# Kernel optimization log

Measured on AMD Instinct MI355X. Metric: run time of the kernel, lower is better.

The kernel has to match this reference:

```python
import jax, jax.numpy as jnp
import numpy as np

DIM = 1536
NUM_HEADS = 24
HEAD_DIM = DIM // NUM_HEADS
SCALE = HEAD_DIM ** -0.5
B, NX, NC = 2, 2048, 256


def setup_inputs() -> dict:
    key = jax.random.key(0)
    ks = jax.random.split(key, 12)
    s = 0.02
    return {
        "x": jax.random.normal(ks[0], (B, NX, DIM), jnp.float32),
        "c": jax.random.normal(ks[1], (B, NC, DIM), jnp.float32),
        "Wqkv_x": jax.random.normal(ks[2], (3 * DIM, DIM), jnp.float32) * s,
        "bqkv_x": jax.random.normal(ks[3], (3 * DIM,), jnp.float32) * s,
        "Wqkv_c": jax.random.normal(ks[4], (3 * DIM, DIM), jnp.float32) * s,
        "bqkv_c": jax.random.normal(ks[5], (3 * DIM,), jnp.float32) * s,
        "Wproj_x": jax.random.normal(ks[6], (DIM, DIM), jnp.float32) * s,
        "bproj_x": jax.random.normal(ks[7], (DIM,), jnp.float32) * s,
        "Wproj_c": jax.random.normal(ks[8], (DIM, DIM), jnp.float32) * s,
        "bproj_c": jax.random.normal(ks[9], (DIM,), jnp.float32) * s,
    }


def _qkv(t, W, b):
    # t: [B, N, C] -> q, k, v each [B, H, N, Dh]
    Bt, N, C = t.shape
    qkv = (t @ W.T + b).reshape(Bt, N, 3, NUM_HEADS, HEAD_DIM)
    qkv = jnp.transpose(qkv, (2, 0, 3, 1, 4))  # [3, B, H, N, Dh]
    return qkv[0], qkv[1], qkv[2]


def reference(x, c, Wqkv_x, bqkv_x, Wqkv_c, bqkv_c, Wproj_x, bproj_x, Wproj_c, bproj_c):
    q_x, k_x, v_x = _qkv(x, Wqkv_x, bqkv_x)
    q_c, k_c, v_c = _qkv(c, Wqkv_c, bqkv_c)
    q = jnp.concatenate([q_x, q_c], axis=2)  # [B, H, Nx+Nc, Dh]
    k = jnp.concatenate([k_x, k_c], axis=2)
    v = jnp.concatenate([v_x, v_c], axis=2)
    attn = jnp.einsum("bhnd,bhmd->bhnm", q, k) * SCALE
    attn = jax.nn.softmax(attn, axis=-1)
    out = jnp.einsum("bhnm,bhmd->bhnd", attn, v)  # [B, H, N, Dh]
    x_out = out[:, :, :NX]
    c_out = out[:, :, NX:]
    x_out = jnp.transpose(x_out, (0, 2, 1, 3)).reshape(x.shape[0], NX, DIM)
    c_out = jnp.transpose(c_out, (0, 2, 1, 3)).reshape(c.shape[0], NC, DIM)
    return (x_out @ Wproj_x.T + bproj_x, c_out @ Wproj_c.T + bproj_c)
```

## Files before the change

### kernel.cpp

```cpp
#include <hip/hip_runtime.h>
#include <stdint.h>

#define HNUM 24
#define DIMX 1536
#define NXT  2048
#define NCT  256
#define NTOT 2304
#define BB   2

typedef __attribute__((ext_vector_type(8))) short bf16x8;
typedef __attribute__((ext_vector_type(8))) _Float16 f16x8;
typedef __attribute__((ext_vector_type(4))) _Float16 f16x4;
typedef __attribute__((ext_vector_type(4))) float f32x4;
typedef __attribute__((ext_vector_type(4))) unsigned short u16x4;

#define AS1 __attribute__((address_space(1)))
#define AS3 __attribute__((address_space(3)))

__device__ __forceinline__ void glds16(const void* g, void* l) {
  __builtin_amdgcn_global_load_lds((AS1 void*)(uintptr_t)g, (AS3 void*)l, 16, 0, 0);
}

__device__ __forceinline__ unsigned short f2bf(float f) {
  unsigned int u = __float_as_uint(f);
  u += 0x7FFFu + ((u >> 16) & 1u);
  return (unsigned short)(u >> 16);
}

__device__ __forceinline__ bf16x8 ldfragB(const unsigned short* S, int row, int cc) {
  return *(const bf16x8*)(S + row * 64 + ((cc ^ (row & 7)) << 3));
}
__device__ __forceinline__ f16x8 ldfragH(const _Float16* S, int row, int cc) {
  return *(const f16x8*)(S + row * 64 + ((cc ^ (row & 7)) << 3));
}

struct CastDesc { const float* src; unsigned short* dst; int start4; };
struct CastArgs { CastDesc d[6]; int total4; };

__global__ __launch_bounds__(256) void cast_all(CastArgs a) {
  int i = blockIdx.x * 256 + threadIdx.x;
  if (i >= a.total4) return;
  int r = 0;
#pragma unroll
  for (int k = 1; k < 6; ++k) r += (i >= a.d[k].start4);
  int j = i - a.d[r].start4;
  float4 v = reinterpret_cast<const float4*>(a.d[r].src)[j];
  u16x4 o;
  o[0] = f2bf(v.x); o[1] = f2bf(v.y); o[2] = f2bf(v.z); o[3] = f2bf(v.w);
  reinterpret_cast<u16x4*>(a.d[r].dst)[j] = o;
}

__device__ __forceinline__ void gemm_mainloop(
    const unsigned short* __restrict__ Ablk,
    const unsigned short* __restrict__ Wblk,
    unsigned short* As, unsigned short* Bs, f32x4 acc[4][4]) {
  const int tid  = threadIdx.x;
  const int lane = tid & 63;
  const int quad = lane >> 4, l16 = lane & 15;
  const int wave = tid >> 6;
  const int wm = (wave >> 1) * 64, wo = (wave & 1) * 64;

  for (int k0 = 0; k0 < DIMX; k0 += 64) {
    __syncthreads();
#pragma unroll
    for (int p = 0; p < 4; ++p) {
      int c = p * 256 + tid;
      int row = c >> 3;
      int kc = ((c & 7) ^ (row & 7)) << 3;
      glds16(Ablk + (size_t)row * DIMX + k0 + kc, As + c * 8);
      glds16(Wblk + (size_t)row * DIMX + k0 + kc, Bs + c * 8);
    }
    __syncthreads();
#pragma unroll
    for (int kk = 0; kk < 64; kk += 32) {
      bf16x8 af[4], bf[4];
#pragma unroll
      for (int mb = 0; mb < 4; ++mb)
        af[mb] = ldfragB(As, wm + mb * 16 + l16, (kk >> 3) + quad);
#pragma unroll
      for (int ob = 0; ob < 4; ++ob)
        bf[ob] = ldfragB(Bs, wo + ob * 16 + l16, (kk >> 3) + quad);
#pragma unroll
      for (int mb = 0; mb < 4; ++mb)
#pragma unroll
        for (int ob = 0; ob < 4; ++ob)
          acc[mb][ob] = __builtin_amdgcn_mfma_f32_16x16x32_bf16(
              af[mb], bf[ob], acc[mb][ob], 0, 0, 0);
    }
  }
}

__global__ __launch_bounds__(256, 3) void gemm_qkv(
    const unsigned short* __restrict__ xbf, const unsigned short* __restrict__ cbf,
    const unsigned short* __restrict__ Wx, const unsigned short* __restrict__ Wc,
    const float* __restrict__ bx_, const float* __restrict__ bc_,
    unsigned short* __restrict__ Qb, unsigned short* __restrict__ Kb,
    _Float16* __restrict__ VTf) {
  __shared__ unsigned short Sh[2][128 * 64];
  unsigned short* As = Sh[0];
  unsigned short* Bs = Sh[1];

  const bool isC = blockIdx.y >= 32;
  const int yloc = isC ? (int)blockIdx.y - 32 : (int)blockIdx.y;
  const int tokShift = isC ? 8 : 11;
  const int seqOff = isC ? NXT : 0;
  const unsigned short* A = (isC ? cbf : xbf) + (size_t)yloc * 128 * DIMX;
  const unsigned short* W = (isC ? Wc : Wx) + (size_t)blockIdx.x * 128 * DIMX;
  const float* bias = isC ? bc_ : bx_;

  const f32x4 z4 = {0.f, 0.f, 0.f, 0.f};
  f32x4 acc[4][4];
#pragma unroll
  for (int i = 0; i < 4; ++i)
#pragma unroll
    for (int j = 0; j < 4; ++j) acc[i][j] = z4;

  gemm_mainloop(A, W, As, Bs, acc);

  const int tid = threadIdx.x, lane = tid & 63, wave = tid >> 6;
  const int quad = lane >> 4, l16 = lane & 15;
  const int wm = (wave >> 1) * 64, wo = (wave & 1) * 64;
  const int s = blockIdx.x / 12;
  const float QSC = 0.125f * 1.44269504088896340736f;

  float bv[4];
#pragma unroll
  for (int ob = 0; ob < 4; ++ob)
    bv[ob] = bias[blockIdx.x * 128 + wo + ob * 16 + l16];

  if (s < 2) {
#pragma unroll
    for (int ob = 0; ob < 4; ++ob) {
      int o = blockIdx.x * 128 + wo + ob * 16 + l16;
      int rem = o - s * DIMX;
      int h = rem >> 6, d = rem & 63;
#pragma unroll
      for (int mb = 0; mb < 4; ++mb) {
#pragma unroll
        for (int r = 0; r < 4; ++r) {
          int m = yloc * 128 + wm + mb * 16 + quad * 4 + r;
          int b = m >> tokShift;
          int n = seqOff + (m & ((1 << tokShift) - 1));
          size_t bh = (size_t)b * HNUM + h;
          float v = acc[mb][ob][r] + bv[ob];
          if (s == 0) Qb[(bh * NTOT + n) * 64 + d] = f2bf(v * QSC);
          else        Kb[(bh * NTOT + n) * 64 + d] = f2bf(v);
        }
      }
    }
  } else {
    _Float16* Ts = (_Float16*)Sh;
    __syncthreads();
#pragma unroll
    for (int ob = 0; ob < 4; ++ob) {
      int dloc = wo + ob * 16 + l16;
      int sw = (dloc & 15) << 3;
#pragma unroll
      for (int mb = 0; mb < 4; ++mb) {
        f16x4 pk;
#pragma unroll
        for (int r = 0; r < 4; ++r) pk[r] = (_Float16)(acc[mb][ob][r] + bv[ob]);
        int m0 = wm + mb * 16 + quad * 4;
        *(f16x4*)(Ts + dloc * 128 + (m0 ^ sw)) = pk;
      }
    }
    __syncthreads();
#pragma unroll
    for (int it = 0; it < 8; ++it) {
      int cth = it * 256 + tid;
      int d = cth >> 4;
      int m0 = (cth & 15) << 3;
      f16x8 val = *(const f16x8*)(Ts + d * 128 + (m0 ^ ((d & 15) << 3)));
      int dglob = (blockIdx.x - 24) * 128 + d;
      int h = dglob >> 6, dd = dglob & 63;
      int M = yloc * 128 + m0;
      int b = M >> tokShift;
      int n = seqOff + (M & ((1 << tokShift) - 1));
      *(f16x8*)(VTf + ((size_t)(b * HNUM + h) * 64 + dd) * NTOT + n) = val;
    }
  }
}

__global__ __launch_bounds__(256, 3) void gemm_proj(
    const unsigned short* __restrict__ AX, const unsigned short* __restrict__ AC,
    const unsigned short* __restrict__ Wx, const unsigned short* __restrict__ Wc,
    const float* __restrict__ bx_, const float* __restrict__ bc_,
    float* __restrict__ out) {
  __shared__ unsigned short As[128 * 64];
  __shared__ unsigned short Bs[128 * 64];

  const bool isC = blockIdx.y >= 32;
  const int yloc = isC ? (int)blockIdx.y - 32 : (int)blockIdx.y;
  const unsigned short* A = (isC ? AC : AX) + (size_t)yloc * 128 * DIMX;
  const unsigned short* W = (isC ? Wc : Wx) + (size_t)blockIdx.x * 128 * DIMX;
  const float* bias = isC ? bc_ : bx_;
  float* o_ = out + (isC ? (size_t)BB * NXT * DIMX : (size_t)0) +
              (size_t)yloc * 128 * DIMX;

  const f32x4 z4 = {0.f, 0.f, 0.f, 0.f};
  f32x4 acc[4][4];
#pragma unroll
  for (int i = 0; i < 4; ++i)
#pragma unroll
    for (int j = 0; j < 4; ++j) acc[i][j] = z4;

  gemm_mainloop(A, W, As, Bs, acc);

  const int lane = threadIdx.x & 63, wave = threadIdx.x >> 6;
  const int quad = lane >> 4, l16 = lane & 15;
  const int wm = (wave >> 1) * 64, wo = (wave & 1) * 64;

#pragma unroll
  for (int ob = 0; ob < 4; ++ob) {
    int o = blockIdx.x * 128 + wo + ob * 16 + l16;
    float bv = bias[o];
#pragma unroll
    for (int mb = 0; mb < 4; ++mb) {
#pragma unroll
      for (int r = 0; r < 4; ++r) {
        int m = wm + mb * 16 + quad * 4 + r;
        o_[(size_t)m * DIMX + o] = acc[mb][ob][r] + bv;
      }
    }
  }
}

__global__ __launch_bounds__(256, 3) void flash_attn(
    const unsigned short* __restrict__ Qb, const unsigned short* __restrict__ Kb,
    const _Float16* __restrict__ Vf,
    unsigned short* __restrict__ AX, unsigned short* __restrict__ AC) {
  __shared__ unsigned short Ks[64 * 64];
  __shared__ _Float16      Vs[64 * 64];
  __shared__ _Float16      Ps[4][32 * 72];

  const int tid = threadIdx.x, lane = tid & 63, wave = tid >> 6;
  const int quad = lane >> 4, l16 = lane & 15;
  const int bh = blockIdx.y;
  const int qbase = blockIdx.x * 128 + wave * 32;

  bf16x8 qf[2][2];
#pragma unroll
  for (int qb = 0; qb < 2; ++qb)
#pragma unroll
    for (int kh = 0; kh < 2; ++kh)
      qf[qb][kh] = *(const bf16x8*)(
          Qb + ((size_t)bh * NTOT + qbase + qb * 16 + l16) * 64 + kh * 32 + quad * 8);

  const f32x4 z4 = {0.f, 0.f, 0.f, 0.f};
  f32x4 acc[2][4];
  float lp[2][4];
#pragma unroll
  for (int qb = 0; qb < 2; ++qb) {
#pragma unroll
    for (int db = 0; db < 4; ++db) acc[qb][db] = z4;
#pragma unroll
    for (int r = 0; r < 4; ++r) lp[qb][r] = 0.f;
  }

  const size_t kbase = (size_t)bh * NTOT * 64;
  const size_t vbase = (size_t)bh * 64 * NTOT;
  _Float16* Pw = &Ps[wave][0];

  for (int kt = 0; kt < 36; ++kt) {
    const int kv0 = kt * 64;
    __syncthreads();
#pragma unroll
    for (int p = 0; p < 2; ++p) {
      int c = p * 256 + tid;
      int row = c >> 3;
      int kc = ((c & 7) ^ (row & 7)) << 3;
      glds16(Kb + kbase + (size_t)(kv0 + row) * 64 + kc, Ks + c * 8);
      glds16(Vf + vbase + (size_t)row * NTOT + kv0 + kc, Vs + c * 8);
    }
    __syncthreads();

    f32x4 s[2][4];
#pragma unroll
    for (int qb = 0; qb < 2; ++qb)
#pragma unroll
      for (int cb = 0; cb < 4; ++cb) s[qb][cb] = z4;
#pragma unroll
    for (int kh = 0; kh < 2; ++kh) {
      bf16x8 kf[4];
#pragma unroll
      for (int cb = 0; cb < 4; ++cb)
        kf[cb] = ldfragB(Ks, cb * 16 + l16, kh * 4 + quad);
#pragma unroll
      for (int qb = 0; qb < 2; ++qb)
#pragma unroll
        for (int cb = 0; cb < 4; ++cb)
          s[qb][cb] = __builtin_amdgcn_mfma_f32_16x16x32_bf16(
              qf[qb][kh], kf[cb], s[qb][cb], 0, 0, 0);
    }

#pragma unroll
    for (int qb = 0; qb < 2; ++qb)
#pragma unroll
      for (int cb = 0; cb < 4; ++cb)
#pragma unroll
        for (int r = 0; r < 4; ++r) {
          float pe = __builtin_amdgcn_exp2f(s[qb][cb][r]);
          lp[qb][r] += pe;
          Pw[(qb * 16 + quad * 4 + r) * 72 + cb * 16 + l16] = (_Float16)pe;
        }

#pragma unroll
    for (int kh = 0; kh < 2; ++kh) {
      f16x8 pf[2];
#pragma unroll
      for (int qb = 0; qb < 2; ++qb)
        pf[qb] = *(const f16x8*)(Pw + (qb * 16 + l16) * 72 + kh * 32 + quad * 8);
#pragma unroll
      for (int db = 0; db < 4; ++db) {
        f16x8 vfr = ldfragH(Vs, db * 16 + l16, kh * 4 + quad);
#pragma unroll
        for (int qb = 0; qb < 2; ++qb)
          acc[qb][db] = __builtin_amdgcn_mfma_f32_16x16x32_f16(
              pf[qb], vfr, acc[qb][db], 0, 0, 0);
      }
    }
  }

  float inv[2][4];
#pragma unroll
  for (int qb = 0; qb < 2; ++qb)
#pragma unroll
    for (int r = 0; r < 4; ++r) {
      float l = lp[qb][r];
      l += __shfl_xor(l, 1);
      l += __shfl_xor(l, 2);
      l += __shfl_xor(l, 4);
      l += __shfl_xor(l, 8);
      inv[qb][r] = __frcp_rn(l);
    }

  const int b = bh / HNUM, h = bh - b * HNUM;
#pragma unroll
  for (int qb = 0; qb < 2; ++qb)
#pragma unroll
    for (int db = 0; db < 4; ++db)
#pragma unroll
      for (int r = 0; r < 4; ++r) {
        int n = qbase + qb * 16 + quad * 4 + r;
        int col = h * 64 + db * 16 + l16;
        unsigned short ov = f2bf(acc[qb][db][r] * inv[qb][r]);
        if (n < NXT) AX[((size_t)b * NXT + n) * DIMX + col] = ov;
        else         AC[((size_t)b * NCT + (n - NXT)) * DIMX + col] = ov;
      }
}

extern "C" void kernel_launch(void* const* d_in, const int* in_sizes, int n_in,
                              void* d_out, int out_size, void* d_ws, size_t ws_size,
                              hipStream_t stream) {
  const float* x       = (const float*)d_in[0];
  const float* c       = (const float*)d_in[1];
  const float* Wqkv_x  = (const float*)d_in[2];
  const float* bqkv_x  = (const float*)d_in[3];
  const float* Wqkv_c  = (const float*)d_in[4];
  const float* bqkv_c  = (const float*)d_in[5];
  const float* Wproj_x = (const float*)d_in[6];
  const float* bproj_x = (const float*)d_in[7];
  const float* Wproj_c = (const float*)d_in[8];
  const float* bproj_c = (const float*)d_in[9];
  float* out = (float*)d_out;

  char* ws = (char*)d_ws;
  size_t off = 0;
  auto alloc = [&](size_t nelem) {
    unsigned short* p = (unsigned short*)(ws + off);
    off += nelem * 2;
    return p;
  };
  unsigned short* xbf  = alloc((size_t)BB * NXT * DIMX);
  unsigned short* cbf  = alloc((size_t)BB * NCT * DIMX);
  unsigned short* wqx  = alloc((size_t)3 * DIMX * DIMX);
  unsigned short* wqc  = alloc((size_t)3 * DIMX * DIMX);
  unsigned short* wpx  = alloc((size_t)DIMX * DIMX);
  unsigned short* wpc  = alloc((size_t)DIMX * DIMX);
  unsigned short* Qb   = alloc((size_t)BB * HNUM * NTOT * 64);
  unsigned short* Kb   = alloc((size_t)BB * HNUM * NTOT * 64);
  _Float16*       VTf  = (_Float16*)alloc((size_t)BB * HNUM * NTOT * 64);
  unsigned short* AX   = alloc((size_t)BB * NXT * DIMX);
  unsigned short* AC   = alloc((size_t)BB * NCT * DIMX);

  CastArgs ca;
  const float* srcs[6] = {x, c, Wqkv_x, Wqkv_c, Wproj_x, Wproj_c};
  unsigned short* dsts[6] = {xbf, cbf, wqx, wqc, wpx, wpc};
  size_t ns[6] = {(size_t)BB * NXT * DIMX, (size_t)BB * NCT * DIMX,
                  (size_t)3 * DIMX * DIMX, (size_t)3 * DIMX * DIMX,
                  (size_t)DIMX * DIMX, (size_t)DIMX * DIMX};
  int acc4 = 0;
  for (int i = 0; i < 6; ++i) {
    ca.d[i].src = srcs[i];
    ca.d[i].dst = dsts[i];
    ca.d[i].start4 = acc4;
    acc4 += (int)(ns[i] / 4);
  }
  ca.total4 = acc4;
  cast_all<<<dim3((acc4 + 255) / 256), dim3(256), 0, stream>>>(ca);

  gemm_qkv<<<dim3(36, 36), dim3(256), 0, stream>>>(xbf, cbf, wqx, wqc,
                                                   bqkv_x, bqkv_c, Qb, Kb, VTf);

  flash_attn<<<dim3(18, 48), dim3(256), 0, stream>>>(Qb, Kb, VTf, AX, AC);

  gemm_proj<<<dim3(12, 36), dim3(256), 0, stream>>>(AX, AC, wpx, wpc,
                                                    bproj_x, bproj_c, out);
}
```

Measured before the change: 358.8 us.

## Double-buffer K/V tiles and keep P in registers via transposed S

```diff
diff --git a/kernel.cpp b/kernel.cpp
--- a/kernel.cpp
+++ b/kernel.cpp
@@ -30,8 +30,10 @@
 __device__ __forceinline__ bf16x8 ldfragB(const unsigned short* S, int row, int cc) {
   return *(const bf16x8*)(S + row * 64 + ((cc ^ (row & 7)) << 3));
 }
-__device__ __forceinline__ f16x8 ldfragH(const _Float16* S, int row, int cc) {
-  return *(const f16x8*)(S + row * 64 + ((cc ^ (row & 7)) << 3));
+__device__ __forceinline__ f16x4 ldVfrag(const _Float16* S, int row, int mb, int quad) {
+  int gc = mb * 2 + (quad >> 1);
+  int cp = gc ^ (row & 7);
+  return *(const f16x4*)(S + row * 64 + cp * 8 + (quad & 1) * 4);
 }
 
 struct CastDesc { const float* src; unsigned short* dst; int start4; };
@@ -229,9 +231,8 @@
     const unsigned short* __restrict__ Qb, const unsigned short* __restrict__ Kb,
     const _Float16* __restrict__ Vf,
     unsigned short* __restrict__ AX, unsigned short* __restrict__ AC) {
-  __shared__ unsigned short Ks[64 * 64];
-  __shared__ _Float16      Vs[64 * 64];
-  __shared__ _Float16      Ps[4][32 * 72];
+  __shared__ unsigned short Ks[2][64 * 64];
+  __shared__ _Float16      Vs[2][64 * 64];
 
   const int tid = threadIdx.x, lane = tid & 63, wave = tid >> 6;
   const int quad = lane >> 4, l16 = lane & 15;
@@ -247,106 +248,104 @@
           Qb + ((size_t)bh * NTOT + qbase + qb * 16 + l16) * 64 + kh * 32 + quad * 8);
 
   const f32x4 z4 = {0.f, 0.f, 0.f, 0.f};
-  f32x4 acc[2][4];
-  float lp[2][4];
-#pragma unroll
-  for (int qb = 0; qb < 2; ++qb) {
-#pragma unroll
-    for (int db = 0; db < 4; ++db) acc[qb][db] = z4;
-#pragma unroll
-    for (int r = 0; r < 4; ++r) lp[qb][r] = 0.f;
-  }
+  f32x4 accT[2][4];
+  float lp[2] = {0.f, 0.f};
+#pragma unroll
+  for (int qb = 0; qb < 2; ++qb)
+#pragma unroll
+    for (int db = 0; db < 4; ++db) accT[qb][db] = z4;
 
   const size_t kbase = (size_t)bh * NTOT * 64;
   const size_t vbase = (size_t)bh * 64 * NTOT;
-  _Float16* Pw = &Ps[wave][0];
-
-  for (int kt = 0; kt < 36; ++kt) {
+
+  auto stage = [&](int kt, int buf) {
     const int kv0 = kt * 64;
-    __syncthreads();
 #pragma unroll
     for (int p = 0; p < 2; ++p) {
       int c = p * 256 + tid;
       int row = c >> 3;
       int kc = ((c & 7) ^ (row & 7)) << 3;
-      glds16(Kb + kbase + (size_t)(kv0 + row) * 64 + kc, Ks + c * 8);
-      glds16(Vf + vbase + (size_t)row * NTOT + kv0 + kc, Vs + c * 8);
-    }
+      glds16(Kb + kbase + (size_t)(kv0 + row) * 64 + kc, &Ks[buf][0] + c * 8);
+      glds16(Vf + vbase + (size_t)row * NTOT + kv0 + kc, &Vs[buf][0] + c * 8);
+    }
+  };
+
+  stage(0, 0);
+  for (int kt = 0; kt < 36; ++kt) {
     __syncthreads();
-
-    f32x4 s[2][4];
+    if (kt < 35) stage(kt + 1, (kt + 1) & 1);
+    const unsigned short* K_ = &Ks[kt & 1][0];
+    const _Float16*       V_ = &Vs[kt & 1][0];
+
+    f32x4 st[2][4];
 #pragma unroll
     for (int qb = 0; qb < 2; ++qb)
 #pragma unroll
-      for (int cb = 0; cb < 4; ++cb) s[qb][cb] = z4;
+      for (int mb = 0; mb < 4; ++mb) st[qb][mb] = z4;
 #pragma unroll
     for (int kh = 0; kh < 2; ++kh) {
-      bf16x8 kf[4];
-#pragma unroll
-      for (int cb = 0; cb < 4; ++cb)
-        kf[cb] = ldfragB(Ks, cb * 16 + l16, kh * 4 + quad);
-#pragma unroll
-      for (int qb = 0; qb < 2; ++qb)
-#pragma unroll
-        for (int cb = 0; cb < 4; ++cb)
-          s[qb][cb] = __builtin_amdgcn_mfma_f32_16x16x32_bf16(
-              qf[qb][kh], kf[cb], s[qb][cb], 0, 0, 0);
-    }
-
+#pragma unroll
+      for (int mb = 0; mb < 4; ++mb) {
+        bf16x8 kf = ldfragB(K_, mb * 16 + l16, kh * 4 + quad);
+#pragma unroll
+        for (int qb = 0; qb < 2; ++qb)
+          st[qb][mb] = __builtin_amdgcn_mfma_f32_16x16x32_bf16(
+              kf, qf[qb][kh], st[qb][mb], 0, 0, 0);
+      }
+    }
+
+    f16x4 pf[2][4];
 #pragma unroll
     for (int qb = 0; qb < 2; ++qb)
 #pragma unroll
-      for (int cb = 0; cb < 4; ++cb)
-#pragma unroll
-        for (int r = 0; r < 4; ++r) {
-          float pe = __builtin_amdgcn_exp2f(s[qb][cb][r]);
-          lp[qb][r] += pe;
-          Pw[(qb * 16 + quad * 4 + r) * 72 + cb * 16 + l16] = (_Float16)pe;
-        }
-
-#pragma unroll
-    for (int kh = 0; kh < 2; ++kh) {
-      f16x8 pf[2];
-#pragma unroll
-      for (int qb = 0; qb < 2; ++qb)
-        pf[qb] = *(const f16x8*)(Pw + (qb * 16 + l16) * 72 + kh * 32 + quad * 8);
-#pragma unroll
-      for (int db = 0; db < 4; ++db) {
-        f16x8 vfr = ldfragH(Vs, db * 16 + l16, kh * 4 + quad);
+      for (int mb = 0; mb < 4; ++mb) {
+        float p0 = __builtin_amdgcn_exp2f(st[qb][mb][0]);
+        float p1 = __builtin_amdgcn_exp2f(st[qb][mb][1]);
+        float p2 = __builtin_amdgcn_exp2f(st[qb][mb][2]);
+        float p3 = __builtin_amdgcn_exp2f(st[qb][mb][3]);
+        lp[qb] += (p0 + p1) + (p2 + p3);
+        f16x4 pk = {(_Float16)p0, (_Float16)p1, (_Float16)p2, (_Float16)p3};
+        pf[qb][mb] = pk;
+      }
+
+#pragma unroll
+    for (int db = 0; db < 4; ++db) {
+#pragma unroll
+      for (int mb = 0; mb < 4; ++mb) {
+        f16x4 vfr = ldVfrag(V_, db * 16 + l16, mb, quad);
 #pragma unroll
         for (int qb = 0; qb < 2; ++qb)
-          acc[qb][db] = __builtin_amdgcn_mfma_f32_16x16x32_f16(
-              pf[qb], vfr, acc[qb][db], 0, 0, 0);
-      }
-    }
-  }
-
-  float inv[2][4];
-#pragma unroll
-  for (int qb = 0; qb < 2; ++qb)
-#pragma unroll
-    for (int r = 0; r < 4; ++r) {
-      float l = lp[qb][r];
-      l += __shfl_xor(l, 1);
-      l += __shfl_xor(l, 2);
-      l += __shfl_xor(l, 4);
-      l += __shfl_xor(l, 8);
-      inv[qb][r] = __frcp_rn(l);
-    }
+          accT[qb][db] = __builtin_amdgcn_mfma_f32_16x16x16f16(
+              vfr, pf[qb][mb], accT[qb][db], 0, 0, 0);
+      }
+    }
+  }
+
+  float inv[2];
+#pragma unroll
+  for (int qb = 0; qb < 2; ++qb) {
+    float l = lp[qb];
+    l += __shfl_xor(l, 16);
+    l += __shfl_xor(l, 32);
+    inv[qb] = __frcp_rn(l);
+  }
 
   const int b = bh / HNUM, h = bh - b * HNUM;
 #pragma unroll
-  for (int qb = 0; qb < 2; ++qb)
-#pragma unroll
-    for (int db = 0; db < 4; ++db)
-#pragma unroll
-      for (int r = 0; r < 4; ++r) {
-        int n = qbase + qb * 16 + quad * 4 + r;
-        int col = h * 64 + db * 16 + l16;
-        unsigned short ov = f2bf(acc[qb][db][r] * inv[qb][r]);
-        if (n < NXT) AX[((size_t)b * NXT + n) * DIMX + col] = ov;
-        else         AC[((size_t)b * NCT + (n - NXT)) * DIMX + col] = ov;
-      }
+  for (int qb = 0; qb < 2; ++qb) {
+    int n = qbase + qb * 16 + l16;
+#pragma unroll
+    for (int db = 0; db < 4; ++db) {
+      u16x4 o;
+#pragma unroll
+      for (int r = 0; r < 4; ++r) o[r] = f2bf(accT[qb][db][r] * inv[qb]);
+      int col = h * 64 + db * 16 + quad * 4;
+      if (n < NXT)
+        *(u16x4*)(AX + ((size_t)b * NXT + n) * DIMX + col) = o;
+      else
+        *(u16x4*)(AC + ((size_t)b * NCT + (n - NXT)) * DIMX + col) = o;
+    }
+  }
 }
 
 extern "C" void kernel_launch(void* const* d_in, const int* in_sizes, int n_in,
```

Measured after the change: 356.7 us. About the same (-0.6%).
